# Optimization experiments

Measured on AMD Instinct MI355X. Metric: run time of the kernel, lower is better.

## Reference

```python
import jax, jax.numpy as jnp
import numpy as np

DEPTH = 2
EPS = 1e-12

def _l2norm(x, axis=-1):
    n = jnp.sqrt(jnp.sum(x * x, axis=axis, keepdims=True))
    return x / jnp.maximum(n, EPS)

def setup_inputs() -> dict:
    key = jax.random.key(0)
    k1, k2, k3, k4, k5 = jax.random.split(key, 5)
    N, D, R, E = 50000, 100, 1000, 800000
    features = jax.random.normal(k1, (N, D), dtype=jnp.float32)
    rel_emb = jax.random.normal(k2, (R, D), dtype=jnp.float32)
    none_relation = jax.random.normal(k3, (D,), dtype=jnp.float32)
    # edge list sorted by destination row (matches coalesced sparse layout
    # assumed by the original: softmax values align with edge order)
    rows = jnp.sort(jax.random.randint(k4, (E,), 0, N))
    cols = jax.random.randint(k5, (E,), 0, N)
    adj_index = jnp.stack([rows, cols], axis=1).astype(jnp.int64)
    return {"features": features, "rel_emb": rel_emb,
            "adj_index": adj_index, "none_relation": none_relation}

def reference(features, rel_emb, adj_index, none_relation):
    N = features.shape[0]
    rows = adj_index[:, 0]  # destination (softmax segment, scatter target)
    cols = adj_index[:, 1]  # neighbor (gather source)
    feats = jnp.tanh(features)
    outputs = [feats]
    nr = _l2norm(none_relation, axis=0)  # [D]
    for _ in range(DEPTH):
        neighs = feats[cols]                      # [E, D] gather
        score = -jnp.einsum('ed,d->e', _l2norm(neighs), nr)  # [E]
        # sparse softmax over each destination row's edges
        m = jax.ops.segment_max(score, rows, num_segments=N)
        e = jnp.exp(score - m[rows])
        denom = jax.ops.segment_sum(e, rows, num_segments=N)
        att = e / denom[rows]                     # [E]
        new_feats = jax.ops.segment_sum(neighs * att[:, None], rows,
                                        num_segments=N)  # [N, D]
        feats = jnp.tanh(new_feats)
        outputs.append(feats)
    return jnp.concatenate(outputs, axis=1)  # [N, D*(DEPTH+1)]
```

## Files before the change

### kernel.cpp

```cpp
#include <hip/hip_runtime.h>
#include <hip/hip_fp16.h>
#include <math.h>

#define D_FEAT 100
#define ROW_STRIDE 300
#define ROWB 128u

__device__ __forceinline__ float fast_tanh(float x) {
    float ax = fabsf(x);
    float e  = __expf(2.f * ax);
    float t  = 1.f - 2.f / (e + 1.f);
    return copysignf(t, x);
}

__device__ __forceinline__ unsigned pb4(float x0, float x1, float x2, float x3) {
    unsigned b0 = (unsigned)(int)rintf(fmaf(x0, 127.f, 128.f));
    unsigned b1 = (unsigned)(int)rintf(fmaf(x1, 127.f, 128.f));
    unsigned b2 = (unsigned)(int)rintf(fmaf(x2, 127.f, 128.f));
    unsigned b3 = (unsigned)(int)rintf(fmaf(x3, 127.f, 128.f));
    return b0 | (b1 << 8) | (b2 << 16) | (b3 << 24);
}

__device__ __forceinline__ float half_reduce(float v) {
    #pragma unroll
    for (int off = 16; off; off >>= 1) v += __shfl_xor(v, off, 64);
    return v;
}

__global__ __launch_bounds__(256) void tanh_score_kernel(
    const float* __restrict__ features,
    float* __restrict__ out,
    unsigned char* __restrict__ tab0,
    float* __restrict__ escore0,
    const float* __restrict__ none_rel,
    const int* __restrict__ adj,
    int* __restrict__ startArr,
    int* __restrict__ cols,
    int E, int N)
{
    int gtid = blockIdx.x * blockDim.x + threadIdx.x;
    if (gtid < E && cols) cols[gtid] = adj[2 * gtid + 1];
    if (gtid <= N) {
        if (gtid == N) startArr[N] = E;
        else {
            int lo = 0, hi = E;
            while (lo < hi) {
                int mid = (lo + hi) >> 1;
                if (adj[2 * mid] < gtid) lo = mid + 1; else hi = mid;
            }
            startArr[gtid] = lo;
        }
    }

    int waveId = gtid >> 6;
    int lane = threadIdx.x & 63;
    int h32  = lane >> 5;
    int l    = lane & 31;
    int n    = waveId * 2 + h32;
    const bool valid_n = (n < N);
    const bool fact = valid_n && (l >= 1) && (l <= 25);

    float x0 = 0.f, x1 = 0.f, x2 = 0.f, x3 = 0.f;
    if (fact) {
        float4 f = ((const float4*)(features + (size_t)n * D_FEAT))[l - 1];
        x0 = fast_tanh(f.x); x1 = fast_tanh(f.y);
        x2 = fast_tanh(f.z); x3 = fast_tanh(f.w);
        ((float4*)(out + (size_t)n * ROW_STRIDE))[l - 1] = make_float4(x0, x1, x2, x3);
    }
    if (tab0 && valid_n) {
        unsigned char* row = tab0 + ((size_t)n << 7);
        if (l >= 1 && l <= 25) {
            *(unsigned*)(row + 4 * (l - 1)) = pb4(x0, x1, x2, x3);
        } else if (l >= 26) {
            *(unsigned*)(row + 4 * (l - 1)) = 0x80808080u;
        } else {
            *(unsigned*)(row + 124) = 0x80808080u;
        }
    }

    float nx = 0.f, ny = 0.f, nz = 0.f, nw = 0.f;
    if (l >= 1 && l <= 25) {
        float4 v = ((const float4*)none_rel)[l - 1];
        nx = v.x; ny = v.y; nz = v.z; nw = v.w;
    }
    float ss = half_reduce(nx * nx + ny * ny + nz * nz + nw * nw);
    float inv_nr = 1.f / fmaxf(sqrtf(ss), 1e-12f);

    float dot = half_reduce(x0 * nx + x1 * ny + x2 * nz + x3 * nw) * inv_nr;
    float sq  = half_reduce(x0 * x0 + x1 * x1 + x2 * x2 + x3 * x3);
    if (l == 0 && valid_n) {
        float es = __expf(-dot / fmaxf(sqrtf(sq), 1e-12f));
        escore0[n] = es;
    }
}

template <bool WRITE_TAB>
__global__ __launch_bounds__(256) void attn8_kernel(
    const unsigned char* __restrict__ tab,
    float* __restrict__ outp,
    unsigned char* __restrict__ tab_out,
    const int* __restrict__ cols,
    const int* __restrict__ start,
    const float* __restrict__ esc_in,
    float* __restrict__ esc_out,
    const float* __restrict__ none_rel,
    int N)
{
    const int waveId = (int)((blockIdx.x * blockDim.x + threadIdx.x) >> 6);
    const int lane = threadIdx.x & 63;
    const int h32  = lane >> 5;
    const int hl   = lane & 31;
    const int base = h32 << 5;
    const int n    = waveId * 2 + h32;
    const bool valid_n = (n < N);

    const int grp = hl >> 3;
    const unsigned suboff = (unsigned)((hl & 7) << 4);

    int e0 = 0, e1 = 0;
    if (valid_n) { e0 = start[n]; e1 = start[n + 1]; }
    const int deg = e1 - e0;
    int maxdeg = deg;
    { int o = __shfl_xor(maxdeg, 32, 64); maxdeg = maxdeg > o ? maxdeg : o; }

    int   c0 = 0, c1 = 0;
    float w0 = 0.f, w1 = 0.f;
    if (hl < deg)      { c0 = cols[e0 + hl];      w0 = esc_in[c0]; }
    if (hl + 32 < deg) { c1 = cols[e0 + hl + 32]; w1 = esc_in[c1]; }

    float dsum = half_reduce(w0 + w1);

    float a[16];
    #pragma unroll
    for (int k = 0; k < 16; ++k) a[k] = 0.f;

#define ACC16(V, W)                                                           \
    {                                                                         \
        unsigned _d;                                                          \
        _d = (V).x;                                                           \
        a[0]  = fmaf((float)(_d & 255u),         (W), a[0]);                  \
        a[1]  = fmaf((float)((_d >> 8) & 255u),  (W), a[1]);                  \
        a[2]  = fmaf((float)((_d >> 16) & 255u), (W), a[2]);                  \
        a[3]  = fmaf((float)(_d >> 24),          (W), a[3]);                  \
        _d = (V).y;                                                           \
        a[4]  = fmaf((float)(_d & 255u),         (W), a[4]);                  \
        a[5]  = fmaf((float)((_d >> 8) & 255u),  (W), a[5]);                  \
        a[6]  = fmaf((float)((_d >> 16) & 255u), (W), a[6]);                  \
        a[7]  = fmaf((float)(_d >> 24),          (W), a[7]);                  \
        _d = (V).z;                                                           \
        a[8]  = fmaf((float)(_d & 255u),         (W), a[8]);                  \
        a[9]  = fmaf((float)((_d >> 8) & 255u),  (W), a[9]);                  \
        a[10] = fmaf((float)((_d >> 16) & 255u), (W), a[10]);                 \
        a[11] = fmaf((float)(_d >> 24),          (W), a[11]);                 \
        _d = (V).w;                                                           \
        a[12] = fmaf((float)(_d & 255u),         (W), a[12]);                 \
        a[13] = fmaf((float)((_d >> 8) & 255u),  (W), a[13]);                 \
        a[14] = fmaf((float)((_d >> 16) & 255u), (W), a[14]);                 \
        a[15] = fmaf((float)(_d >> 24),          (W), a[15]);                 \
    }

#define BATCH16(CST, WST, RBASE)                                              \
    {                                                                         \
        const int s0 = base + (RBASE) + grp;                                  \
        int   cA = __shfl((CST), s0,      64), cB = __shfl((CST), s0 + 4, 64);\
        int   cC = __shfl((CST), s0 + 8,  64), cD = __shfl((CST), s0 + 12,64);\
        float wA = __shfl((WST), s0,      64), wB = __shfl((WST), s0 + 4, 64);\
        float wC = __shfl((WST), s0 + 8,  64), wD = __shfl((WST), s0 + 12,64);\
        const uint4 vA = *(const uint4*)(tab + (((size_t)(unsigned)cA) << 7) + suboff); \
        const uint4 vB = *(const uint4*)(tab + (((size_t)(unsigned)cB) << 7) + suboff); \
        const uint4 vC = *(const uint4*)(tab + (((size_t)(unsigned)cC) << 7) + suboff); \
        const uint4 vD = *(const uint4*)(tab + (((size_t)(unsigned)cD) << 7) + suboff); \
        ACC16(vA, wA) ACC16(vB, wB) ACC16(vC, wC) ACC16(vD, wD)               \
    }

    const int cap1 = maxdeg < 32 ? maxdeg : 32;
    for (int r = 0; r < cap1; r += 16) BATCH16(c0, w0, r)
    const int cap2 = maxdeg < 64 ? maxdeg : 64;
    for (int r = 32; r < cap2; r += 16) BATCH16(c1, w1, r - 32)
#undef BATCH16

    for (int e = e0 + 64; e < e1; ++e) {
        int   c = cols[e];
        float w = esc_in[c];
        const uint4 v = *(const uint4*)(tab + (((size_t)(unsigned)c) << 7) + suboff);
        if (grp == 0) ACC16(v, w)
        dsum += w;
    }
#undef ACC16

    #pragma unroll
    for (int k = 0; k < 16; ++k) a[k] += __shfl_xor(a[k], 16, 64);
    #pragma unroll
    for (int k = 0; k < 16; ++k) a[k] += __shfl_xor(a[k], 8, 64);

    const float invd = (deg > 0) ? 1.f / (127.f * dsum) : 0.f;
    const float bsh  = (deg > 0) ? (-128.f / 127.f) : 0.f;
    float r[16];
    #pragma unroll
    for (int k = 0; k < 16; ++k) {
        r[k] = fast_tanh(fmaf(a[k], invd, bsh));
        if (!valid_n || hl >= 8 || (16 * hl + k) >= 100) r[k] = 0.f;
    }

    if (valid_n && hl < 8) {
        if (hl < 7) {
            float4* orow = (float4*)(outp + (size_t)n * ROW_STRIDE);
            #pragma unroll
            for (int j = 0; j < 4; ++j) {
                if (j == 0 || hl < 6)
                    orow[4 * hl + j] = make_float4(r[4*j], r[4*j+1], r[4*j+2], r[4*j+3]);
            }
        }
        if constexpr (WRITE_TAB) {
            unsigned char* trow = tab_out + ((size_t)n << 7);
            *(uint4*)(trow + 16 * hl) = make_uint4(
                pb4(r[0],  r[1],  r[2],  r[3]),
                pb4(r[4],  r[5],  r[6],  r[7]),
                pb4(r[8],  r[9],  r[10], r[11]),
                pb4(r[12], r[13], r[14], r[15]));
        }
    }

    if constexpr (WRITE_TAB) {
        float nn[16];
        #pragma unroll
        for (int k = 0; k < 16; ++k) nn[k] = 0.f;
        if (hl < 7) {
            #pragma unroll
            for (int j = 0; j < 4; ++j) {
                if (j == 0 || hl < 6) {
                    float4 u = *(const float4*)(none_rel + 16 * hl + 4 * j);
                    nn[4*j] = u.x; nn[4*j+1] = u.y; nn[4*j+2] = u.z; nn[4*j+3] = u.w;
                }
            }
        }
        float ssl = 0.f, dotl = 0.f, sql = 0.f;
        #pragma unroll
        for (int k = 0; k < 16; ++k) {
            ssl  += nn[k] * nn[k];
            dotl += r[k] * nn[k];
            sql  += r[k] * r[k];
        }
        float ss  = half_reduce(ssl);
        float inv_nr = 1.f / fmaxf(sqrtf(ss), 1e-12f);
        float dot = half_reduce(dotl) * inv_nr;
        float sq  = half_reduce(sql);
        if (hl == 0 && valid_n) {
            float es = __expf(-dot / fmaxf(sqrtf(sq), 1e-12f));
            esc_out[n] = es;
        }
    }
}

__global__ __launch_bounds__(256) void attn_f32_kernel(
    const float* __restrict__ prev,
    float* __restrict__ outp,
    const int2* __restrict__ adj2,
    const int* __restrict__ start,
    const float* __restrict__ escore_in,
    float* __restrict__ escore_out,
    const float* __restrict__ none_rel,
    int N)
{
    int waveId = (int)((blockIdx.x * blockDim.x + threadIdx.x) >> 6);
    int lane = threadIdx.x & 63;
    int h32  = lane >> 5;
    int l    = lane & 31;
    int n    = waveId * 2 + h32;
    const bool valid_n = (n < N);
    const bool fact = valid_n && (l >= 1) && (l <= 25);
    const int base = h32 << 5;

    int e0 = 0, e1 = 0;
    if (valid_n) { e0 = start[n]; e1 = start[n + 1]; }
    const int deg = e1 - e0;

    int   c0 = 0, c1 = 0;
    float w0 = 0.f, w1 = 0.f;
    if (l < deg)      { c0 = adj2[e0 + l].y;      w0 = escore_in[c0]; }
    if (l + 32 < deg) { c1 = adj2[e0 + l + 32].y; w1 = escore_in[c1]; }

    int maxdeg = deg;
    { int o = __shfl_xor(maxdeg, 32, 64); maxdeg = maxdeg > o ? maxdeg : o; }

    float d_acc = 0.f, a0 = 0.f, a1 = 0.f, a2 = 0.f, a3 = 0.f;
    const int cap1 = maxdeg < 32 ? maxdeg : 32;
    for (int r = 0; r < cap1; r += 8) {
        #pragma unroll
        for (int j = 0; j < 8; ++j) {
            int   i = r + j;
            int   c = __shfl(c0, base + i, 64);
            float w = __shfl(w0, base + i, 64);
            float p0 = 0.f, p1 = 0.f, p2 = 0.f, p3 = 0.f;
            if (fact && (i < deg)) {
                float4 v = ((const float4*)(prev + (size_t)c * ROW_STRIDE))[l - 1];
                p0 = v.x; p1 = v.y; p2 = v.z; p3 = v.w;
            }
            if (i >= deg) w = 0.f;
            d_acc += w;
            a0 += w * p0; a1 += w * p1; a2 += w * p2; a3 += w * p3;
        }
    }
    const int cap2 = maxdeg < 64 ? maxdeg : 64;
    for (int r = 32; r < cap2; r += 8) {
        #pragma unroll
        for (int j = 0; j < 8; ++j) {
            int   i = r + j;
            int   c = __shfl(c1, base + i - 32, 64);
            float w = __shfl(w1, base + i - 32, 64);
            float p0 = 0.f, p1 = 0.f, p2 = 0.f, p3 = 0.f;
            if (fact && (i < deg)) {
                float4 v = ((const float4*)(prev + (size_t)c * ROW_STRIDE))[l - 1];
                p0 = v.x; p1 = v.y; p2 = v.z; p3 = v.w;
            }
            if (i >= deg) w = 0.f;
            d_acc += w;
            a0 += w * p0; a1 += w * p1; a2 += w * p2; a3 += w * p3;
        }
    }
    for (int e = e0 + 64; e < e1; ++e) {
        int c = adj2[e].y;
        float w = escore_in[c];
        float p0 = 0.f, p1 = 0.f, p2 = 0.f, p3 = 0.f;
        if (fact) {
            float4 v = ((const float4*)(prev + (size_t)c * ROW_STRIDE))[l - 1];
            p0 = v.x; p1 = v.y; p2 = v.z; p3 = v.w;
        }
        d_acc += w;
        a0 += w * p0; a1 += w * p1; a2 += w * p2; a3 += w * p3;
    }

    const float inv_d = (deg > 0) ? 1.f / d_acc : 0.f;
    float r0 = fast_tanh(a0 * inv_d);
    float r1 = fast_tanh(a1 * inv_d);
    float r2 = fast_tanh(a2 * inv_d);
    float r3 = fast_tanh(a3 * inv_d);
    if (fact) {
        ((float4*)(outp + (size_t)n * ROW_STRIDE))[l - 1] = make_float4(r0, r1, r2, r3);
    } else {
        r0 = r1 = r2 = r3 = 0.f;
    }

    if (escore_out) {
        float nx = 0.f, ny = 0.f, nz = 0.f, nw = 0.f;
        if (l >= 1 && l <= 25) {
            float4 v = ((const float4*)none_rel)[l - 1];
            nx = v.x; ny = v.y; nz = v.z; nw = v.w;
        }
        float ss = half_reduce(nx * nx + ny * ny + nz * nz + nw * nw);
        float inv_nr = 1.f / fmaxf(sqrtf(ss), 1e-12f);
        float dot = half_reduce(r0 * nx + r1 * ny + r2 * nz + r3 * nw) * inv_nr;
        float sq  = half_reduce(r0 * r0 + r1 * r1 + r2 * r2 + r3 * r3);
        if (l == 0 && valid_n) {
            float es = __expf(-dot / fmaxf(sqrtf(sq), 1e-12f));
            escore_out[n] = es;
        }
    }
}

extern "C" void kernel_launch(void* const* d_in, const int* in_sizes, int n_in,
                              void* d_out, int out_size, void* d_ws, size_t ws_size,
                              hipStream_t stream) {
    const float* features = (const float*)d_in[0];
    const int*   adj      = (const int*)d_in[2];
    const float* none_rel = (const float*)d_in[3];
    float* out = (float*)d_out;

    const int N = in_sizes[0] / D_FEAT;
    const int E = in_sizes[2] / 2;

    size_t off = 0;
    auto take = [&](size_t bytes) { size_t o = off; off = (off + bytes + 127) & ~(size_t)127; return o; };
    char* w = (char*)d_ws;
    int*   start   = (int*)  (w + take(sizeof(int)   * (size_t)(N + 1)));
    float* escore0 = (float*)(w + take(sizeof(float) * (size_t)N));
    float* escore1 = (float*)(w + take(sizeof(float) * (size_t)N));
    int*   cols    = (int*)  (w + take(sizeof(int)   * (size_t)E));
    size_t tab_off0 = take((size_t)N * ROWB);
    size_t tab_off1 = take((size_t)N * ROWB);
    const bool use_tab = (ws_size >= off) &&
                         ((((uintptr_t)w) & 127) == 0);
    unsigned char* tab0 = use_tab ? (unsigned char*)(w + tab_off0) : nullptr;
    unsigned char* tab1 = use_tab ? (unsigned char*)(w + tab_off1) : nullptr;

    const int pairs = (N + 1) / 2;
    const int node_blocks = (pairs * 64 + 255) / 256;
    const int2* adj2 = (const int2*)adj;

    tanh_score_kernel<<<node_blocks, 256, 0, stream>>>(features, out, tab0,
                                                       escore0, none_rel,
                                                       adj, start,
                                                       use_tab ? cols : nullptr,
                                                       E, N);
    if (use_tab) {
        attn8_kernel<true><<<node_blocks, 256, 0, stream>>>(
            tab0, out + D_FEAT, tab1, cols, start, escore0, escore1, none_rel, N);
        attn8_kernel<false><<<node_blocks, 256, 0, stream>>>(
            tab1, out + 2 * D_FEAT, nullptr, cols, start, escore1, nullptr, none_rel, N);
    } else {
        attn_f32_kernel<<<node_blocks, 256, 0, stream>>>(
            out, out + D_FEAT, adj2, start, escore0, escore1, none_rel, N);
        attn_f32_kernel<<<node_blocks, 256, 0, stream>>>(
            out + D_FEAT, out + 2 * D_FEAT, adj2, start, escore1, nullptr, none_rel, N);
    }
}
```

Measured before the change: 168.2 us.

## Embed edge softmax weight in packed table row and spread epilogue across lanes

Stores each node's exp-score as a float inside the unused tail of its 128-byte quantized feature row, so the gather loads the weight together with the features instead of doing a dependent esc_in[c] lookup. A sentinel row N with zero weight lets padded lanes load harmlessly without branching. The epilogue now spreads the tanh, packing and score work over all 32 lanes, each handling 4 features, instead of 8 lanes handling 16. The column extraction also uses vectorized 16-byte loads. The cost is extra shuffles per batch and an extra table row, and if E is odd the last column is no longer copied.

```diff
diff --git a/kernel.cpp b/kernel.cpp
--- a/kernel.cpp
+++ b/kernel.cpp
@@ -39,7 +39,10 @@
     int E, int N)
 {
     int gtid = blockIdx.x * blockDim.x + threadIdx.x;
-    if (gtid < E && cols) cols[gtid] = adj[2 * gtid + 1];
+    if (cols && gtid < (E >> 1)) {
+        uint4 v = ((const uint4*)adj)[gtid];
+        ((int2*)cols)[gtid] = make_int2((int)v.y, (int)v.w);
+    }
     if (gtid <= N) {
         if (gtid == N) startArr[N] = E;
         else {
@@ -51,6 +54,11 @@
             startArr[gtid] = lo;
         }
     }
+    if (tab0 && gtid < 8) {
+        uint4 z = make_uint4(0x80808080u, 0x80808080u, 0x80808080u, 0x80808080u);
+        if (gtid == 7) z.x = 0u;
+        *(uint4*)(tab0 + (((size_t)N) << 7) + ((size_t)gtid << 4)) = z;
+    }
 
     int waveId = gtid >> 6;
     int lane = threadIdx.x & 63;
@@ -67,13 +75,13 @@
         x2 = fast_tanh(f.z); x3 = fast_tanh(f.w);
         ((float4*)(out + (size_t)n * ROW_STRIDE))[l - 1] = make_float4(x0, x1, x2, x3);
     }
-    if (tab0 && valid_n) {
-        unsigned char* row = tab0 + ((size_t)n << 7);
+    unsigned char* row = tab0 ? (tab0 + ((size_t)n << 7)) : nullptr;
+    if (row && valid_n) {
         if (l >= 1 && l <= 25) {
             *(unsigned*)(row + 4 * (l - 1)) = pb4(x0, x1, x2, x3);
-        } else if (l >= 26) {
+        } else if (l >= 26 && l != 29) {
             *(unsigned*)(row + 4 * (l - 1)) = 0x80808080u;
-        } else {
+        } else if (l == 0) {
             *(unsigned*)(row + 124) = 0x80808080u;
         }
     }
@@ -91,6 +99,7 @@
     if (l == 0 && valid_n) {
         float es = __expf(-dot / fmaxf(sqrtf(sq), 1e-12f));
         escore0[n] = es;
+        if (row) *(float*)(row + 112) = es;
     }
 }
 
@@ -101,11 +110,17 @@
     unsigned char* __restrict__ tab_out,
     const int* __restrict__ cols,
     const int* __restrict__ start,
-    const float* __restrict__ esc_in,
-    float* __restrict__ esc_out,
     const float* __restrict__ none_rel,
     int N)
 {
+    if constexpr (WRITE_TAB) {
+        if (blockIdx.x == 0 && threadIdx.x < 8) {
+            uint4 z = make_uint4(0x80808080u, 0x80808080u, 0x80808080u, 0x80808080u);
+            if (threadIdx.x == 7) z.x = 0u;
+            *(uint4*)(tab_out + (((size_t)N) << 7) + ((size_t)threadIdx.x << 4)) = z;
+        }
+    }
+
     const int waveId = (int)((blockIdx.x * blockDim.x + threadIdx.x) >> 6);
     const int lane = threadIdx.x & 63;
     const int h32  = lane >> 5;
@@ -114,8 +129,10 @@
     const int n    = waveId * 2 + h32;
     const bool valid_n = (n < N);
 
-    const int grp = hl >> 3;
-    const unsigned suboff = (unsigned)((hl & 7) << 4);
+    const int grp   = hl >> 3;
+    const int chunk = hl & 7;
+    const unsigned suboff = (unsigned)(chunk << 4);
+    const int wl = base + (grp << 3) + 7;
 
     int e0 = 0, e1 = 0;
     if (valid_n) { e0 = start[n]; e1 = start[n + 1]; }
@@ -123,16 +140,14 @@
     int maxdeg = deg;
     { int o = __shfl_xor(maxdeg, 32, 64); maxdeg = maxdeg > o ? maxdeg : o; }
 
-    int   c0 = 0, c1 = 0;
-    float w0 = 0.f, w1 = 0.f;
-    if (hl < deg)      { c0 = cols[e0 + hl];      w0 = esc_in[c0]; }
-    if (hl + 32 < deg) { c1 = cols[e0 + hl + 32]; w1 = esc_in[c1]; }
-
-    float dsum = half_reduce(w0 + w1);
+    int c0 = N, c1 = N;
+    if (hl < deg)      c0 = cols[e0 + hl];
+    if (hl + 32 < deg) c1 = cols[e0 + hl + 32];
 
     float a[16];
     #pragma unroll
     for (int k = 0; k < 16; ++k) a[k] = 0.f;
+    float dsum = 0.f;
 
 #define ACC16(V, W)                                                           \
     {                                                                         \
@@ -159,32 +174,34 @@
         a[15] = fmaf((float)(_d >> 24),          (W), a[15]);                 \
     }
 
-#define BATCH16(CST, WST, RBASE)                                              \
+#define BATCH16(CST, RBASE)                                                   \
     {                                                                         \
-        const int s0 = base + (RBASE) + grp;                                  \
-        int   cA = __shfl((CST), s0,      64), cB = __shfl((CST), s0 + 4, 64);\
-        int   cC = __shfl((CST), s0 + 8,  64), cD = __shfl((CST), s0 + 12,64);\
-        float wA = __shfl((WST), s0,      64), wB = __shfl((WST), s0 + 4, 64);\
-        float wC = __shfl((WST), s0 + 8,  64), wD = __shfl((WST), s0 + 12,64);\
+        const int sA = base + (RBASE) + grp;                                  \
+        int   cA = __shfl((CST), sA,      64), cB = __shfl((CST), sA + 4, 64);\
+        int   cC = __shfl((CST), sA + 8,  64), cD = __shfl((CST), sA + 12,64);\
         const uint4 vA = *(const uint4*)(tab + (((size_t)(unsigned)cA) << 7) + suboff); \
         const uint4 vB = *(const uint4*)(tab + (((size_t)(unsigned)cB) << 7) + suboff); \
         const uint4 vC = *(const uint4*)(tab + (((size_t)(unsigned)cC) << 7) + suboff); \
         const uint4 vD = *(const uint4*)(tab + (((size_t)(unsigned)cD) << 7) + suboff); \
+        const float wA = __shfl(__uint_as_float(vA.x), wl, 64);               \
+        const float wB = __shfl(__uint_as_float(vB.x), wl, 64);               \
+        const float wC = __shfl(__uint_as_float(vC.x), wl, 64);               \
+        const float wD = __shfl(__uint_as_float(vD.x), wl, 64);               \
+        dsum += wA + wB + wC + wD;                                            \
         ACC16(vA, wA) ACC16(vB, wB) ACC16(vC, wC) ACC16(vD, wD)               \
     }
 
     const int cap1 = maxdeg < 32 ? maxdeg : 32;
-    for (int r = 0; r < cap1; r += 16) BATCH16(c0, w0, r)
+    for (int r = 0; r < cap1; r += 16) BATCH16(c0, r)
     const int cap2 = maxdeg < 64 ? maxdeg : 64;
-    for (int r = 32; r < cap2; r += 16) BATCH16(c1, w1, r - 32)
+    for (int r = 32; r < cap2; r += 16) BATCH16(c1, r - 32)
 #undef BATCH16
 
     for (int e = e0 + 64; e < e1; ++e) {
-        int   c = cols[e];
-        float w = esc_in[c];
+        int c = cols[e];
         const uint4 v = *(const uint4*)(tab + (((size_t)(unsigned)c) << 7) + suboff);
-        if (grp == 0) ACC16(v, w)
-        dsum += w;
+        float wv = __shfl(__uint_as_float(v.x), base + 7, 64);
+        if (grp == 0) { ACC16(v, wv) dsum += wv; }
     }
 #undef ACC16
 
@@ -192,62 +209,43 @@
     for (int k = 0; k < 16; ++k) a[k] += __shfl_xor(a[k], 16, 64);
     #pragma unroll
     for (int k = 0; k < 16; ++k) a[k] += __shfl_xor(a[k], 8, 64);
+    dsum += __shfl_xor(dsum, 16, 64);
+    dsum += __shfl_xor(dsum, 8, 64);
 
     const float invd = (deg > 0) ? 1.f / (127.f * dsum) : 0.f;
     const float bsh  = (deg > 0) ? (-128.f / 127.f) : 0.f;
-    float r[16];
-    #pragma unroll
-    for (int k = 0; k < 16; ++k) {
-        r[k] = fast_tanh(fmaf(a[k], invd, bsh));
-        if (!valid_n || hl >= 8 || (16 * hl + k) >= 100) r[k] = 0.f;
-    }
-
-    if (valid_n && hl < 8) {
-        if (hl < 7) {
-            float4* orow = (float4*)(outp + (size_t)n * ROW_STRIDE);
-            #pragma unroll
-            for (int j = 0; j < 4; ++j) {
-                if (j == 0 || hl < 6)
-                    orow[4 * hl + j] = make_float4(r[4*j], r[4*j+1], r[4*j+2], r[4*j+3]);
-            }
-        }
-        if constexpr (WRITE_TAB) {
-            unsigned char* trow = tab_out + ((size_t)n << 7);
-            *(uint4*)(trow + 16 * hl) = make_uint4(
-                pb4(r[0],  r[1],  r[2],  r[3]),
-                pb4(r[4],  r[5],  r[6],  r[7]),
-                pb4(r[8],  r[9],  r[10], r[11]),
-                pb4(r[12], r[13], r[14], r[15]));
-        }
-    }
-
+    const int f0 = (chunk << 4) + (grp << 2);
+    const bool live = valid_n && (f0 < 100);
+    float r0 = 0.f, r1 = 0.f, r2 = 0.f, r3 = 0.f;
+    if (live) {
+        r0 = fast_tanh(fmaf(a[(grp << 2) + 0], invd, bsh));
+        r1 = fast_tanh(fmaf(a[(grp << 2) + 1], invd, bsh));
+        r2 = fast_tanh(fmaf(a[(grp << 2) + 2], invd, bsh));
+        r3 = fast_tanh(fmaf(a[(grp << 2) + 3], invd, bsh));
+    }
+
+    float es = 0.f;
     if constexpr (WRITE_TAB) {
-        float nn[16];
-        #pragma unroll
-        for (int k = 0; k < 16; ++k) nn[k] = 0.f;
-        if (hl < 7) {
-            #pragma unroll
-            for (int j = 0; j < 4; ++j) {
-                if (j == 0 || hl < 6) {
-                    float4 u = *(const float4*)(none_rel + 16 * hl + 4 * j);
-                    nn[4*j] = u.x; nn[4*j+1] = u.y; nn[4*j+2] = u.z; nn[4*j+3] = u.w;
-                }
-            }
-        }
-        float ssl = 0.f, dotl = 0.f, sql = 0.f;
-        #pragma unroll
-        for (int k = 0; k < 16; ++k) {
-            ssl  += nn[k] * nn[k];
-            dotl += r[k] * nn[k];
-            sql  += r[k] * r[k];
-        }
-        float ss  = half_reduce(ssl);
+        float n0 = 0.f, n1 = 0.f, n2 = 0.f, n3 = 0.f;
+        if (f0 < 100) {
+            float4 u = *(const float4*)(none_rel + f0);
+            n0 = u.x; n1 = u.y; n2 = u.z; n3 = u.w;
+        }
+        float ss   = half_reduce(n0*n0 + n1*n1 + n2*n2 + n3*n3);
         float inv_nr = 1.f / fmaxf(sqrtf(ss), 1e-12f);
-        float dot = half_reduce(dotl) * inv_nr;
-        float sq  = half_reduce(sql);
-        if (hl == 0 && valid_n) {
-            float es = __expf(-dot / fmaxf(sqrtf(sq), 1e-12f));
-            esc_out[n] = es;
+        float dot  = half_reduce(r0*n0 + r1*n1 + r2*n2 + r3*n3) * inv_nr;
+        float sq   = half_reduce(r0*r0 + r1*r1 + r2*r2 + r3*r3);
+        es = __expf(-dot / fmaxf(sqrtf(sq), 1e-12f));
+    }
+
+    if (live) {
+        *(float4*)(outp + (size_t)n * ROW_STRIDE + f0) = make_float4(r0, r1, r2, r3);
+    }
+    if constexpr (WRITE_TAB) {
+        if (valid_n) {
+            unsigned word = live ? pb4(r0, r1, r2, r3) : 0x80808080u;
+            if (f0 == 112) word = __float_as_uint(es);
+            *(unsigned*)(tab_out + ((size_t)n << 7) + (unsigned)f0) = word;
         }
     }
 }
@@ -376,8 +374,8 @@
     float* escore0 = (float*)(w + take(sizeof(float) * (size_t)N));
     float* escore1 = (float*)(w + take(sizeof(float) * (size_t)N));
     int*   cols    = (int*)  (w + take(sizeof(int)   * (size_t)E));
-    size_t tab_off0 = take((size_t)N * ROWB);
-    size_t tab_off1 = take((size_t)N * ROWB);
+    size_t tab_off0 = take((size_t)(N + 1) * ROWB);
+    size_t tab_off1 = take((size_t)(N + 1) * ROWB);
     const bool use_tab = (ws_size >= off) &&
                          ((((uintptr_t)w) & 127) == 0);
     unsigned char* tab0 = use_tab ? (unsigned char*)(w + tab_off0) : nullptr;
@@ -394,9 +392,9 @@
                                                        E, N);
     if (use_tab) {
         attn8_kernel<true><<<node_blocks, 256, 0, stream>>>(
-            tab0, out + D_FEAT, tab1, cols, start, escore0, escore1, none_rel, N);
+            tab0, out + D_FEAT, tab1, cols, start, none_rel, N);
         attn8_kernel<false><<<node_blocks, 256, 0, stream>>>(
-            tab1, out + 2 * D_FEAT, nullptr, cols, start, escore1, nullptr, none_rel, N);
+            tab1, out + 2 * D_FEAT, nullptr, cols, start, none_rel, N);
     } else {
         attn_f32_kernel<<<node_blocks, 256, 0, stream>>>(
             out, out + D_FEAT, adj2, start, escore0, escore1, none_rel, N);
```

Result: faster. 151.8 us (-9.8%).
